# Kernel optimization log

Hardware: AMD Instinct MI355X
Metric: run time of the kernel (lower is better)

## Reference

```python
import jax, jax.numpy as jnp
import numpy as np

N_NODES = 100000
N_EDGES = 3200000
D = 128


def setup_inputs() -> dict:
    key = jax.random.key(0)
    k1, k2, k3, k4, k5 = jax.random.split(key, 5)
    x = jax.random.normal(k1, (N_NODES, D), dtype=jnp.float32)
    weight = jax.random.normal(k2, (D, D), dtype=jnp.float32) * (1.0 / np.sqrt(D))
    bias = jax.random.normal(k3, (D,), dtype=jnp.float32) * 0.01
    edge_weight = jax.random.uniform(k4, (N_EDGES,), dtype=jnp.float32)
    edge_index = jax.random.randint(k5, (2, N_EDGES), 0, N_NODES, dtype=jnp.int64 if jax.config.jax_enable_x64 else jnp.int32)
    return {"x": x, "weight": weight, "bias": bias,
            "edge_weight": edge_weight, "edge_index": edge_index}


def gcn_conv(x, weight, bias, edge_index, edge_weight):
    # PyG GCNConv defaults: normalize=True, add_self_loops=True (fill=1),
    # flow source_to_target: messages gathered from edge_index[0], scattered to edge_index[1].
    n = x.shape[0]
    src, dst = edge_index[0], edge_index[1]
    loop = jnp.arange(n, dtype=src.dtype)
    src = jnp.concatenate([src, loop])
    dst = jnp.concatenate([dst, loop])
    ew = jnp.concatenate([edge_weight, jnp.ones((n,), dtype=edge_weight.dtype)])
    deg = jax.ops.segment_sum(ew, dst, num_segments=n)          # [N]
    dinv = jnp.where(deg > 0, jax.lax.rsqrt(jnp.where(deg > 0, deg, 1.0)), 0.0)
    norm = dinv[src] * ew * dinv[dst]                           # [E+N]
    h = x @ weight.T                                            # [N, D_out]
    msg = h[src] * norm[:, None]                                # gather + scale
    out = jax.ops.segment_sum(msg, dst, num_segments=n)         # scatter-add
    return out + bias


def reference(x, weight, bias, edge_weight, edge_index):
    h = gcn_conv(x, weight, bias, edge_index, edge_weight)
    h = jax.nn.relu(h)            # normalizer is Identity, activation=F.relu
    h = h + x                     # input_dim == output_dim -> projection=Identity
    # dropout: eval mode (deterministic reference) -> no-op
    return h
```

## Files before the change

### kernel.cpp

```cpp
#include <hip/hip_runtime.h>

#define N_NODES 100000
#define N_EDGES 3200000
#define DIM 128

#define NB_C  98
#define CAP_C 36864
#define NB_F  1568
#define CAP_F 2560
#define CAP   96


typedef __attribute__((ext_vector_type(4))) float f32x4;
typedef __attribute__((ext_vector_type(8))) short s16x8;


__device__ __forceinline__ unsigned short f2bf(float f) {
    unsigned u = __float_as_uint(f);
    return (unsigned short)((u + 0x7fffu + ((u >> 16) & 1u)) >> 16);
}


__global__ __launch_bounds__(256) void zero_i_kernel(int* __restrict__ p, int n) {
    int i = blockIdx.x * 256 + threadIdx.x;
    if (i < n) p[i] = 0;
}

__global__ __launch_bounds__(256) void zero_f_kernel(float* __restrict__ p, int n) {
    int i = blockIdx.x * 256 + threadIdx.x;
    if (i < n) p[i] = 0.0f;
}

__global__ __launch_bounds__(256) void zero_u64_kernel(unsigned long long* __restrict__ p, int n) {
    int i = blockIdx.x * 256 + threadIdx.x;
    if (i < n) p[i] = 0ull;
}

__global__ __launch_bounds__(256) void zero_f4_kernel(float4* __restrict__ p, int n4) {
    int i = blockIdx.x * 256 + threadIdx.x;
    if (i < n4) p[i] = make_float4(0.f, 0.f, 0.f, 0.f);
}

__global__ __launch_bounds__(256) void dinv_kernel(float* __restrict__ deg) {
    int i = blockIdx.x * 256 + threadIdx.x;
    if (i < N_NODES) deg[i] = rsqrtf(deg[i] + 1.0f);
}

__global__ __launch_bounds__(256) void dinv_packed_kernel(const unsigned long long* __restrict__ packed,
                                                          float* __restrict__ dinv) {
    int i = blockIdx.x * 256 + threadIdx.x;
    if (i < N_NODES) {
        unsigned long long p = packed[i];
        float deg = (float)(p & 0xFFFFFFFFFFull) * (1.0f / 4294967296.0f);
        dinv[i] = rsqrtf(deg + 1.0f);
    }
}

__global__ __launch_bounds__(256) void wt_kernel(const float* __restrict__ W,
                                                 float* __restrict__ Wt) {
    int idx = blockIdx.x * 256 + threadIdx.x;
    int j = idx >> 7, k = idx & 127;
    Wt[k * 128 + j] = W[idx];
}


__global__ __launch_bounds__(256) void prep_kernel(const float* __restrict__ W,
                                                   ushort* __restrict__ wf_hi,
                                                   ushort* __restrict__ wf_lo,
                                                   int* __restrict__ fills) {
    const int b = blockIdx.x;
    const int tid = threadIdx.x;
    if (b < 64) {
        int idx  = b * 256 + tid;
        int j    = idx & 7;
        int lane = (idx >> 3) & 63;
        int ks   = (idx >> 9) & 3;
        int ct   = idx >> 11;
        int col  = ct * 16 + (lane & 15);
        int k    = ks * 32 + ((lane >> 4) << 3) + j;
        float w  = W[col * 128 + k];
        unsigned short hb = f2bf(w);
        float rem = w - __uint_as_float((unsigned)hb << 16);
        wf_hi[idx] = hb;
        wf_lo[idx] = f2bf(rem);
    } else {
        int i = (b - 64) * 256 + tid;
        if (i < NB_C + NB_F) fills[i] = 0;
    }
}


__global__ __launch_bounds__(256) void partA1_kernel(const int* __restrict__ ei,
                                                     const float* __restrict__ ew,
                                                     int* __restrict__ fill_c,
                                                     unsigned long long* __restrict__ edc) {
    __shared__ int hist[NB_C];
    __shared__ int base[NB_C];
    const int tid = threadIdx.x;
    const int blockbase = blockIdx.x * 4096;
    for (int i = tid; i < NB_C; i += 256) hist[i] = 0;
    __syncthreads();

    unsigned long long pay[16];
    unsigned meta[16];
#pragma unroll
    for (int i = 0; i < 16; ++i) {
        int e = blockbase + i * 256 + tid;
        meta[i] = 0xFFFFFFFFu;
        if (e < N_EDGES) {
            int src = ei[e];
            int dst = ei[N_EDGES + e];
            float w = ew[e];
            int cb = dst >> 10;
            int pos = atomicAdd(&hist[cb], 1);
            pay[i] = ((unsigned long long)__float_as_uint(w) << 32)
                   | ((unsigned)(dst & 1023) << 17) | (unsigned)src;
            meta[i] = ((unsigned)cb << 16) | (unsigned)pos;
        }
    }
    __syncthreads();
    for (int c = tid; c < NB_C; c += 256) {
        int cnt = hist[c];
        base[c] = (cnt > 0) ? atomicAdd(&fill_c[c], cnt) : 0;
    }
    __syncthreads();
#pragma unroll
    for (int i = 0; i < 16; ++i) {
        if (meta[i] != 0xFFFFFFFFu) {
            int cb = (int)(meta[i] >> 16);
            int pos = base[cb] + (int)(meta[i] & 0xFFFFu);
            if (pos < CAP_C)
                edc[(unsigned)cb * CAP_C + (unsigned)pos] = pay[i];
        }
    }
}


__global__ __launch_bounds__(256) void partA2_kernel(const int* __restrict__ fill_c,
                                                     const unsigned long long* __restrict__ edc,
                                                     int* __restrict__ fill_f,
                                                     unsigned long long* __restrict__ edf) {
    __shared__ int hist[16];
    __shared__ int base[16];
    const int tid = threadIdx.x;
    const int cb = blockIdx.x / 9;
    const int lo = (blockIdx.x % 9) * 4096;
    const int cnt_c = min(fill_c[cb], CAP_C);
    const int hi = min(lo + 4096, cnt_c);
    if (tid < 16) hist[tid] = 0;
    __syncthreads();

    unsigned long long pay[16];
    unsigned meta[16];
#pragma unroll
    for (int i = 0; i < 16; ++i) {
        int idx = lo + i * 256 + tid;
        meta[i] = 0xFFFFFFFFu;
        if (idx < hi) {
            unsigned long long p = edc[(unsigned)cb * CAP_C + (unsigned)idx];
            int f = (int)((p >> 23) & 15);
            int pos = atomicAdd(&hist[f], 1);
            pay[i] = p;
            meta[i] = ((unsigned)f << 16) | (unsigned)pos;
        }
    }
    __syncthreads();
    if (tid < 16) {
        int c = hist[tid];
        base[tid] = (c > 0) ? atomicAdd(&fill_f[cb * 16 + tid], c) : 0;
    }
    __syncthreads();
#pragma unroll
    for (int i = 0; i < 16; ++i) {
        if (meta[i] != 0xFFFFFFFFu) {
            int f = (int)(meta[i] >> 16);
            int pos = base[f] + (int)(meta[i] & 0xFFFFu);
            if (pos < CAP_F)
                edf[((unsigned)(cb * 16 + f)) * CAP_F + (unsigned)pos] = pay[i];
        }
    }
}


__global__ __launch_bounds__(256) void partB_kernel(const int* __restrict__ fill_f,
                                                    unsigned long long* __restrict__ edf,
                                                    float* __restrict__ dinv,
                                                    int* __restrict__ row_start,
                                                    int* __restrict__ row_cnt,
                                                    const float4* __restrict__ x4,
                                                    ushort4* __restrict__ xh4) {
    __shared__ unsigned long long hd[64];
    __shared__ int pref[64];
    __shared__ float dinv_s[64];
    const int tid = threadIdx.x;
    const int fb = blockIdx.x;
    const int node_base = fb * 64;
    const int cnt = min(fill_f[fb], CAP_F);
    if (tid < 64) hd[tid] = 0ull;
    __syncthreads();

    unsigned long long pay[10];
    unsigned meta[10];
#pragma unroll
    for (int it = 0; it < 10; ++it) {
        int idx = it * 256 + tid;
        meta[it] = 0xFFFFFFFFu;
        if (idx < cnt) {
            unsigned long long p = edf[(unsigned)fb * CAP_F + (unsigned)idx];
            int dl = (int)((p >> 17) & 63);
            float w = __uint_as_float((unsigned)(p >> 32));
            unsigned long long inc = 1ull |
                ((unsigned long long)(unsigned)(w * 16777216.0f + 0.5f) << 32);
            unsigned long long old = atomicAdd(&hd[dl], inc);
            pay[it] = p;
            meta[it] = ((unsigned)dl << 16) | (unsigned)(old & 0xFFFFull);
        }
    }
    __syncthreads();
    if (tid == 0) {
        int run = 0;
#pragma unroll
        for (int n = 0; n < 64; ++n) { pref[n] = run; run += (int)(hd[n] & 0xFFFFFFFFull); }
    }
    __syncthreads();
    if (tid < 64) {
        int node = node_base + tid;
        if (node < N_NODES) {
            float deg = (float)(unsigned)(hd[tid] >> 32) * (1.0f / 16777216.0f);
            float dv = rsqrtf(deg + 1.0f);
            dinv[node] = dv;
            dinv_s[tid] = dv;
            row_start[node] = fb * CAP_F + pref[tid];
            row_cnt[node] = (int)(hd[tid] & 0xFFFFFFFFull);
        }
    }
#pragma unroll
    for (int it = 0; it < 10; ++it) {
        if (meta[it] != 0xFFFFFFFFu) {
            int dl = (int)(meta[it] >> 16);
            edf[(unsigned)fb * CAP_F + (unsigned)(pref[dl] + (int)(meta[it] & 0xFFFFu))] = pay[it];
        }
    }
    __syncthreads();
#pragma unroll
    for (int i = 0; i < 8; ++i) {
        int idx = i * 256 + tid;
        int r = idx >> 5;
        int node = node_base + r;
        if (node < N_NODES) {
            float dv = dinv_s[r];
            float4 v = x4[(unsigned)node * 32u + (unsigned)(idx & 31)];
            ushort4 h;
            h.x = f2bf(v.x * dv); h.y = f2bf(v.y * dv);
            h.z = f2bf(v.z * dv); h.w = f2bf(v.w * dv);
            xh4[(unsigned)node * 32u + (unsigned)(idx & 31)] = h;
        }
    }
}


__global__ __launch_bounds__(256) void gatherc_kernel(const int* __restrict__ row_start,
                                                      const int* __restrict__ row_cnt,
                                                      const unsigned long long* __restrict__ edf,
                                                      const float* __restrict__ dinv,
                                                      const unsigned* __restrict__ xh,
                                                      float2* __restrict__ agg2) {
    const int lane = threadIdx.x & 63;
    const int node = blockIdx.x * 4 + (threadIdx.x >> 6);

    const int cnt = row_cnt[node];
    const int start = row_start[node];
    float ax0 = 0.f, ay0 = 0.f, ax1 = 0.f, ay1 = 0.f;

    for (int b = 0; b < cnt; b += 64) {
        int idx = b + lane;
        const bool valid = idx < cnt;
        if (!valid) idx = cnt - 1;
        unsigned long long p = edf[(unsigned)(start + idx)];
        int msrc = (int)(p & 0x1FFFFull);
        float mw = valid ? __uint_as_float((unsigned)(p >> 32)) : 0.0f;
        const int mcnt = min(64, cnt - b);
        const int ng = (mcnt + 7) >> 3;

        unsigned va[8], vb[8];

#define PREF(buf, JB)                                                          \
        _Pragma("unroll")                                                      \
        for (int j = 0; j < 8; ++j) {                                          \
            int s = __builtin_amdgcn_readlane(msrc, (JB) + j);                 \
            buf[j] = xh[(unsigned)s * 64u + (unsigned)lane];                   \
        }
#define CONSUME(buf, JB)                                                       \
        _Pragma("unroll")                                                      \
        for (int j = 0; j < 8; ++j) {                                          \
            float w = __int_as_float(                                          \
                __builtin_amdgcn_readlane(__float_as_int(mw), (JB) + j));      \
            if (j & 1) {                                                       \
                ax1 = fmaf(__uint_as_float(buf[j] << 16), w, ax1);             \
                ay1 = fmaf(__uint_as_float(buf[j] & 0xffff0000u), w, ay1);     \
            } else {                                                           \
                ax0 = fmaf(__uint_as_float(buf[j] << 16), w, ax0);             \
                ay0 = fmaf(__uint_as_float(buf[j] & 0xffff0000u), w, ay0);     \
            }                                                                  \
        }

        PREF(va, 0);
        int g = 0;
        for (; g + 2 < ng; g += 2) {
            PREF(vb, (g + 1) * 8);
            CONSUME(va, g * 8);
            PREF(va, (g + 2) * 8);
            CONSUME(vb, (g + 1) * 8);
        }
        if (g + 1 < ng) {
            PREF(vb, (g + 1) * 8);
            CONSUME(va, g * 8);
            CONSUME(vb, (g + 1) * 8);
        } else {
            CONSUME(va, g * 8);
        }
#undef PREF
#undef CONSUME
    }

    float di = dinv[node];
    agg2[(unsigned)node * 64u + lane] = make_float2((ax0 + ax1) * di, (ay0 + ay1) * di);
}


__global__ __launch_bounds__(256) void bucket_f32_kernel(const int* __restrict__ ei,
                                                         const float* __restrict__ ew,
                                                         unsigned long long* __restrict__ packed,
                                                         int2* __restrict__ ed) {
    int e = blockIdx.x * 256 + threadIdx.x;
    int src = ei[e];
    int dst = ei[N_EDGES + e];
    float w = ew[e];
    unsigned long long inc = (1ull << 40) | (unsigned long long)(w * 4294967296.0f);
    unsigned long long old = atomicAdd(&packed[dst], inc);
    unsigned slot = (unsigned)(old >> 40);
    if (slot < CAP) {
        ed[(unsigned)dst * CAP + slot] = make_int2(src, __float_as_int(w));
    }
}

__global__ __launch_bounds__(256) void gatherb_f32_kernel(const unsigned long long* __restrict__ packed,
                                                          const int2* __restrict__ ed,
                                                          const float* __restrict__ dinv,
                                                          const float2* __restrict__ x2,
                                                          float2* __restrict__ agg2) {
    const int wave = threadIdx.x >> 6;
    const int lane = threadIdx.x & 63;
    const int node = blockIdx.x * 4 + wave;

    int cnt = (int)(packed[node] >> 40);
    cnt = min(cnt, CAP);
    const unsigned base = (unsigned)node * CAP;
    float2 acc = make_float2(0.f, 0.f);

    for (int b = 0; b < cnt; b += 64) {
        int idx = b + lane;
        if (idx >= cnt) idx = cnt - 1;
        int2 my = ed[base + idx];
        float wmy = __int_as_float(my.y) * dinv[my.x];
        int m = min(64, cnt - b);
#pragma unroll 8
        for (int j = 0; j < m; ++j) {
            int s = __builtin_amdgcn_readlane(my.x, j);
            float w = __int_as_float(__builtin_amdgcn_readlane(__float_as_int(wmy), j));
            float2 v = x2[(unsigned)s * 64u + lane];
            acc.x = fmaf(v.x, w, acc.x); acc.y = fmaf(v.y, w, acc.y);
        }
    }
    float di = dinv[node];
    acc.x *= di; acc.y *= di;
    agg2[(unsigned)node * 64u + lane] = acc;
}

__global__ __launch_bounds__(256) void count_deg_kernel(const int* __restrict__ ei,
                                                        const float* __restrict__ ew,
                                                        int* __restrict__ count,
                                                        float* __restrict__ deg) {
    int e = blockIdx.x * 256 + threadIdx.x;
    int dst = ei[N_EDGES + e];
    atomicAdd(&count[dst], 1);
    atomicAdd(&deg[dst], ew[e]);
}

__global__ __launch_bounds__(256) void scatter_kernel(const int* __restrict__ ei,
                                                      const float* __restrict__ ew,
                                                      const float* __restrict__ dinv,
                                                      const float4* __restrict__ x4,
                                                      float* __restrict__ agg) {
    unsigned gid = blockIdx.x * 256u + threadIdx.x;
    unsigned e  = gid >> 5;
    unsigned f4 = gid & 31u;
    int src = ei[e];
    int dst = ei[N_EDGES + e];
    float w = dinv[src] * ew[e] * dinv[dst];
    float4 v = x4[(unsigned)src * 32u + f4];
    float* o = agg + ((unsigned)dst * 128u + f4 * 4u);
    atomicAdd(o + 0, v.x * w);
    atomicAdd(o + 1, v.y * w);
    atomicAdd(o + 2, v.z * w);
    atomicAdd(o + 3, v.w * w);
}


__global__ __launch_bounds__(256) void final_mfma_kernel(const float* __restrict__ agg_in,
                                                         const float* __restrict__ x,
                                                         const float* __restrict__ bias,
                                                         const float* __restrict__ dinv,
                                                         const ushort* __restrict__ wf_hi,
                                                         const ushort* __restrict__ wf_lo,
                                                         float* __restrict__ out) {
    __shared__ ushort sh_hi[16384];
    __shared__ ushort sh_lo[16384];
    const int tid = threadIdx.x;
    {
        const float4* sh4 = (const float4*)wf_hi;
        const float4* sl4 = (const float4*)wf_lo;
        float4* dh = (float4*)sh_hi;
        float4* dl = (float4*)sh_lo;
#pragma unroll
        for (int i = 0; i < 8; ++i) {
            dh[i * 256 + tid] = sh4[i * 256 + tid];
            dl[i * 256 + tid] = sl4[i * 256 + tid];
        }
    }
    __syncthreads();

    const int wave = tid >> 6;
    const int lane = tid & 63;
    const int r0 = blockIdx.x * 64 + wave * 16;
    const int mrow = lane & 15;
    const int kg = lane >> 4;
    const int arow = min(r0 + mrow, N_NODES - 1);
    const float di = dinv[arow];
    const float di2 = di * di;

    s16x8 ah[4], al[4];
#pragma unroll
    for (int ks = 0; ks < 4; ++ks) {
        const float* ap = agg_in + (unsigned)arow * 128u + ks * 32 + kg * 8;
        const float* xp = x      + (unsigned)arow * 128u + ks * 32 + kg * 8;
        float4 a0 = *(const float4*)ap;
        float4 a1 = *(const float4*)(ap + 4);
        float4 x0 = *(const float4*)xp;
        float4 x1 = *(const float4*)(xp + 4);
        float v[8] = {a0.x + x0.x * di2, a0.y + x0.y * di2,
                      a0.z + x0.z * di2, a0.w + x0.w * di2,
                      a1.x + x1.x * di2, a1.y + x1.y * di2,
                      a1.z + x1.z * di2, a1.w + x1.w * di2};
        s16x8 h, l;
#pragma unroll
        for (int j = 0; j < 8; ++j) {
            unsigned short hb = f2bf(v[j]);
            h[j] = (short)hb;
            l[j] = (short)f2bf(v[j] - __uint_as_float((unsigned)hb << 16));
        }
        ah[ks] = h; al[ks] = l;
    }

#pragma unroll
    for (int ct = 0; ct < 8; ++ct) {
        f32x4 acc = {0.f, 0.f, 0.f, 0.f};
#pragma unroll
        for (int ks = 0; ks < 4; ++ks) {
            const int fo = ((ct * 4 + ks) * 64 + lane) * 8;
            s16x8 bh = *(const s16x8*)&sh_hi[fo];
            s16x8 bl = *(const s16x8*)&sh_lo[fo];
            acc = __builtin_amdgcn_mfma_f32_16x16x32_bf16(ah[ks], bh, acc, 0, 0, 0);
            acc = __builtin_amdgcn_mfma_f32_16x16x32_bf16(ah[ks], bl, acc, 0, 0, 0);
            acc = __builtin_amdgcn_mfma_f32_16x16x32_bf16(al[ks], bh, acc, 0, 0, 0);
        }
        const int col = ct * 16 + mrow;
        const float bv = bias[col];
#pragma unroll
        for (int v = 0; v < 4; ++v) {
            const int row = r0 + kg * 4 + v;
            if (row < N_NODES) {
                float o = fmaxf(acc[v] + bv, 0.f) + x[(unsigned)row * 128u + col];
                out[(unsigned)row * 128u + col] = o;
            }
        }
    }
}


__global__ __launch_bounds__(256) void final_kernel(const float* __restrict__ agg_in,
                                                    const float* __restrict__ x,
                                                    const float* __restrict__ bias,
                                                    const float* __restrict__ dinv,
                                                    const float* __restrict__ Wt,
                                                    float* __restrict__ out) {
    __shared__ float sh_wt[16384];
    const int tid = threadIdx.x;
    {
        const float4* s4 = (const float4*)Wt;
        float4* d4 = (float4*)sh_wt;
#pragma unroll
        for (int i = 0; i < 16; ++i) d4[i * 256 + tid] = s4[i * 256 + tid];
    }
    __syncthreads();

    const int wave = tid >> 6;
    const int lane = tid & 63;
    const int rowbase = blockIdx.x * 32 + wave * 8;

    float areg[16];
#pragma unroll
    for (int r = 0; r < 8; ++r) {
        int row = rowbase + r;
        float di = dinv[row];
        float di2 = di * di;
        int base = row * 128;
        areg[2 * r]     = agg_in[base + lane]      + x[base + lane]      * di2;
        areg[2 * r + 1] = agg_in[base + 64 + lane] + x[base + 64 + lane] * di2;
    }

    float acc0[8], acc1[8];
#pragma unroll
    for (int r = 0; r < 8; ++r) { acc0[r] = 0.f; acc1[r] = 0.f; }

    const float2* wt2 = (const float2*)sh_wt;

#pragma unroll
    for (int kh = 0; kh < 2; ++kh) {
#pragma unroll 16
        for (int kk = 0; kk < 64; ++kk) {
            int k = kh * 64 + kk;
            float2 w = wt2[k * 64 + lane];
#pragma unroll
            for (int r = 0; r < 8; ++r) {
                float ak = __uint_as_float(
                    __builtin_amdgcn_readlane(__float_as_uint(areg[2 * r + kh]), kk));
                acc0[r] = fmaf(ak, w.x, acc0[r]);
                acc1[r] = fmaf(ak, w.y, acc1[r]);
            }
        }
    }

    float2 b = ((const float2*)bias)[lane];
#pragma unroll
    for (int r = 0; r < 8; ++r) {
        int row = rowbase + r;
        float2 xr = ((const float2*)x)[row * 64 + lane];
        float v0 = fmaxf(acc0[r] + b.x, 0.f) + xr.x;
        float v1 = fmaxf(acc1[r] + b.y, 0.f) + xr.y;
        ((float2*)out)[row * 64 + lane] = make_float2(v0, v1);
    }
}


extern "C" void kernel_launch(void* const* d_in, const int* in_sizes, int n_in,
                              void* d_out, int out_size, void* d_ws, size_t ws_size,
                              hipStream_t stream) {
    const float* x    = (const float*)d_in[0];
    const float* W    = (const float*)d_in[1];
    const float* bias = (const float*)d_in[2];
    const float* ew   = (const float*)d_in[3];
    const int*   ei   = (const int*)d_in[4];
    float* out = (float*)d_out;
    char* ws = (char*)d_ws;

    unsigned short* xhA  = (unsigned short*)ws;
    ushort* wfhi     = (ushort*)(ws + 25600000);
    ushort* wflo     = wfhi + 16384;
    float* dinvA     = (float*)(ws + 25665536);
    int*   row_start = (int*)  (ws + 26065536);
    int*   row_cnt   = (int*)  (ws + 26465536);
    int*   fill_c    = (int*)  (ws + 26865536);
    int*   fill_f    = fill_c + NB_C;
    unsigned long long* edc = (unsigned long long*)(ws + 26872256);
    unsigned long long* edf = (unsigned long long*)(ws + 55773632);
    const size_t WS_PART = 87886272ull;

    unsigned long long* packed = (unsigned long long*)ws;
    float* dinvB = (float*)(ws + 800000);
    float* WtB   = (float*)(ws + 1200000);
    int2*  edB   = (int2*)(ws + 1265536);
    const size_t WS_BUCKET = 1265536ull + (size_t)N_NODES * CAP * 8ull;

    if (ws_size >= WS_PART) {
        prep_kernel<<<71, 256, 0, stream>>>(W, wfhi, wflo, fill_c);
        partA1_kernel<<<(N_EDGES + 4095) / 4096, 256, 0, stream>>>(ei, ew, fill_c, edc);
        partA2_kernel<<<NB_C * 9, 256, 0, stream>>>(fill_c, edc, fill_f, edf);
        partB_kernel<<<NB_F, 256, 0, stream>>>(fill_f, edf, dinvA, row_start, row_cnt,
                                               (const float4*)x, (ushort4*)xhA);
        gatherc_kernel<<<N_NODES / 4, 256, 0, stream>>>(row_start, row_cnt, edf, dinvA,
                                                        (const unsigned*)xhA, (float2*)out);
        final_mfma_kernel<<<(N_NODES + 63) / 64, 256, 0, stream>>>(out, x, bias, dinvA,
                                                                   wfhi, wflo, out);
    } else if (ws_size >= WS_BUCKET) {
        zero_u64_kernel<<<(N_NODES + 255) / 256, 256, 0, stream>>>(packed, N_NODES);
        wt_kernel<<<64, 256, 0, stream>>>(W, WtB);
        bucket_f32_kernel<<<N_EDGES / 256, 256, 0, stream>>>(ei, ew, packed, edB);
        dinv_packed_kernel<<<(N_NODES + 255) / 256, 256, 0, stream>>>(packed, dinvB);
        gatherb_f32_kernel<<<N_NODES / 4, 256, 0, stream>>>(packed, edB, dinvB,
                                                            (const float2*)x, (float2*)out);
        final_kernel<<<N_NODES / 32, 256, 0, stream>>>(out, x, bias, dinvB, WtB, out);
    } else {
        float* deg   = (float*)(ws);
        float* Wt    = (float*)(ws + 400000);
        int*   count = (int*)  (ws + 465536);
        zero_f_kernel<<<(N_NODES + 255) / 256, 256, 0, stream>>>(deg, N_NODES);
        zero_i_kernel<<<(N_NODES + 255) / 256, 256, 0, stream>>>(count, N_NODES);
        wt_kernel<<<64, 256, 0, stream>>>(W, Wt);
        zero_f4_kernel<<<(N_NODES * DIM / 4) / 256, 256, 0, stream>>>((float4*)out,
                                                                      N_NODES * DIM / 4);
        count_deg_kernel<<<N_EDGES / 256, 256, 0, stream>>>(ei, ew, count, deg);
        dinv_kernel<<<(N_NODES + 255) / 256, 256, 0, stream>>>(deg);
        scatter_kernel<<<(N_EDGES / 256) * 32, 256, 0, stream>>>(ei, ew, deg,
                                                                 (const float4*)x, out);
        final_kernel<<<N_NODES / 32, 256, 0, stream>>>(out, x, bias, deg, Wt, out);
    }
}
```

Measured before the change: 351.7 us.

## Replace two-level edge partition with single 256-node bucket pass and staged writes

The three-stage bucketing of edges by destination (1024-node coarse buckets, then 64-node fine buckets, then per-node sort) becomes two stages. A1 now bins edges into 391 buckets of 256 nodes and stages them contiguously in shared memory so the global writes come out grouped per bucket. partB2 then does the per-node histogram and sort directly for each 256-node bucket, and one full pass over the edge list goes away. The final MFMA kernel also stops copying the split-bf16 weights into LDS and reads them straight from global memory. The cost is fewer, larger blocks in partB2 (391), serial loops over up to about 9k edges per block, and B-fragment loads that now depend on cache.

```diff
diff --git a/kernel.cpp b/kernel.cpp
--- a/kernel.cpp
+++ b/kernel.cpp
@@ -4,10 +4,8 @@
 #define N_EDGES 3200000
 #define DIM 128
 
-#define NB_C  98
-#define CAP_C 36864
-#define NB_F  1568
-#define CAP_F 2560
+#define NB2   391
+#define CAP2  9216
 #define CAP   96
 
 
@@ -85,7 +83,7 @@
         wf_lo[idx] = f2bf(rem);
     } else {
         int i = (b - 64) * 256 + tid;
-        if (i < NB_C + NB_F) fills[i] = 0;
+        if (i < NB2) fills[i] = 0;
     }
 }
 
@@ -94,11 +92,15 @@
                                                      const float* __restrict__ ew,
                                                      int* __restrict__ fill_c,
                                                      unsigned long long* __restrict__ edc) {
-    __shared__ int hist[NB_C];
-    __shared__ int base[NB_C];
+    __shared__ int hist[NB2];
+    __shared__ int base[NB2];
+    __shared__ int lpref[NB2 + 1];
+    __shared__ int stripe[98];
+    __shared__ unsigned long long stage[4096];
+    __shared__ unsigned short segid[4096];
     const int tid = threadIdx.x;
     const int blockbase = blockIdx.x * 4096;
-    for (int i = tid; i < NB_C; i += 256) hist[i] = 0;
+    for (int i = tid; i < NB2; i += 256) hist[i] = 0;
     __syncthreads();
 
     unsigned long long pay[16];
@@ -111,139 +113,138 @@
             int src = ei[e];
             int dst = ei[N_EDGES + e];
             float w = ew[e];
-            int cb = dst >> 10;
+            int cb = dst >> 8;
             int pos = atomicAdd(&hist[cb], 1);
             pay[i] = ((unsigned long long)__float_as_uint(w) << 32)
-                   | ((unsigned)(dst & 1023) << 17) | (unsigned)src;
+                   | ((unsigned)(dst & 255) << 17) | (unsigned)src;
             meta[i] = ((unsigned)cb << 16) | (unsigned)pos;
         }
     }
     __syncthreads();
-    for (int c = tid; c < NB_C; c += 256) {
+    for (int c = tid; c < NB2; c += 256) {
         int cnt = hist[c];
         base[c] = (cnt > 0) ? atomicAdd(&fill_c[c], cnt) : 0;
+    }
+    if (tid < 98) {
+        int s = 0;
+#pragma unroll
+        for (int k = 0; k < 4; ++k) { int c = tid * 4 + k; if (c < NB2) s += hist[c]; }
+        stripe[tid] = s;
+    }
+    __syncthreads();
+    if (tid == 0) {
+        int run = 0;
+#pragma unroll
+        for (int i = 0; i < 98; ++i) { int t = stripe[i]; stripe[i] = run; run += t; }
+        lpref[NB2] = run;
+    }
+    __syncthreads();
+    if (tid < 98) {
+        int run = stripe[tid];
+#pragma unroll
+        for (int k = 0; k < 4; ++k) {
+            int c = tid * 4 + k;
+            if (c < NB2) { lpref[c] = run; run += hist[c]; }
+        }
     }
     __syncthreads();
 #pragma unroll
     for (int i = 0; i < 16; ++i) {
         if (meta[i] != 0xFFFFFFFFu) {
             int cb = (int)(meta[i] >> 16);
-            int pos = base[cb] + (int)(meta[i] & 0xFFFFu);
-            if (pos < CAP_C)
-                edc[(unsigned)cb * CAP_C + (unsigned)pos] = pay[i];
-        }
-    }
-}
-
-
-__global__ __launch_bounds__(256) void partA2_kernel(const int* __restrict__ fill_c,
+            int slot = lpref[cb] + (int)(meta[i] & 0xFFFFu);
+            stage[slot] = pay[i];
+            segid[slot] = (unsigned short)cb;
+        }
+    }
+    __syncthreads();
+    const int total = lpref[NB2];
+#pragma unroll
+    for (int r = 0; r < 16; ++r) {
+        int i = r * 256 + tid;
+        if (i < total) {
+            int sid = segid[i];
+            int g = base[sid] + (i - lpref[sid]);
+            if (g < CAP2)
+                edc[(unsigned)sid * CAP2 + (unsigned)g] = stage[i];
+        }
+    }
+}
+
+
+__global__ __launch_bounds__(256) void partB2_kernel(const int* __restrict__ fill_c,
                                                      const unsigned long long* __restrict__ edc,
-                                                     int* __restrict__ fill_f,
-                                                     unsigned long long* __restrict__ edf) {
-    __shared__ int hist[16];
-    __shared__ int base[16];
-    const int tid = threadIdx.x;
-    const int cb = blockIdx.x / 9;
-    const int lo = (blockIdx.x % 9) * 4096;
-    const int cnt_c = min(fill_c[cb], CAP_C);
-    const int hi = min(lo + 4096, cnt_c);
-    if (tid < 16) hist[tid] = 0;
-    __syncthreads();
-
-    unsigned long long pay[16];
-    unsigned meta[16];
-#pragma unroll
-    for (int i = 0; i < 16; ++i) {
-        int idx = lo + i * 256 + tid;
-        meta[i] = 0xFFFFFFFFu;
-        if (idx < hi) {
-            unsigned long long p = edc[(unsigned)cb * CAP_C + (unsigned)idx];
-            int f = (int)((p >> 23) & 15);
-            int pos = atomicAdd(&hist[f], 1);
-            pay[i] = p;
-            meta[i] = ((unsigned)f << 16) | (unsigned)pos;
-        }
-    }
-    __syncthreads();
-    if (tid < 16) {
-        int c = hist[tid];
-        base[tid] = (c > 0) ? atomicAdd(&fill_f[cb * 16 + tid], c) : 0;
-    }
-    __syncthreads();
-#pragma unroll
-    for (int i = 0; i < 16; ++i) {
-        if (meta[i] != 0xFFFFFFFFu) {
-            int f = (int)(meta[i] >> 16);
-            int pos = base[f] + (int)(meta[i] & 0xFFFFu);
-            if (pos < CAP_F)
-                edf[((unsigned)(cb * 16 + f)) * CAP_F + (unsigned)pos] = pay[i];
-        }
-    }
-}
-
-
-__global__ __launch_bounds__(256) void partB_kernel(const int* __restrict__ fill_f,
-                                                    unsigned long long* __restrict__ edf,
-                                                    float* __restrict__ dinv,
-                                                    int* __restrict__ row_start,
-                                                    int* __restrict__ row_cnt,
-                                                    const float4* __restrict__ x4,
-                                                    ushort4* __restrict__ xh4) {
-    __shared__ unsigned long long hd[64];
-    __shared__ int pref[64];
-    __shared__ float dinv_s[64];
+                                                     unsigned long long* __restrict__ edf,
+                                                     float* __restrict__ dinv,
+                                                     int* __restrict__ row_start,
+                                                     int* __restrict__ row_cnt,
+                                                     const float4* __restrict__ x4,
+                                                     ushort4* __restrict__ xh4) {
+    __shared__ unsigned long long hd[256];
+    __shared__ int pref[256];
+    __shared__ int alloc_[256];
+    __shared__ int stripe[64];
+    __shared__ float dinv_s[256];
     const int tid = threadIdx.x;
     const int fb = blockIdx.x;
-    const int node_base = fb * 64;
-    const int cnt = min(fill_f[fb], CAP_F);
-    if (tid < 64) hd[tid] = 0ull;
-    __syncthreads();
-
-    unsigned long long pay[10];
-    unsigned meta[10];
-#pragma unroll
-    for (int it = 0; it < 10; ++it) {
-        int idx = it * 256 + tid;
-        meta[it] = 0xFFFFFFFFu;
-        if (idx < cnt) {
-            unsigned long long p = edf[(unsigned)fb * CAP_F + (unsigned)idx];
-            int dl = (int)((p >> 17) & 63);
-            float w = __uint_as_float((unsigned)(p >> 32));
-            unsigned long long inc = 1ull |
-                ((unsigned long long)(unsigned)(w * 16777216.0f + 0.5f) << 32);
-            unsigned long long old = atomicAdd(&hd[dl], inc);
-            pay[it] = p;
-            meta[it] = ((unsigned)dl << 16) | (unsigned)(old & 0xFFFFull);
-        }
+    const int node_base = fb * 256;
+    const int cnt = min(fill_c[fb], CAP2);
+    const unsigned ebase = (unsigned)fb * CAP2;
+    hd[tid] = 0ull;
+    __syncthreads();
+
+    for (int idx = tid; idx < cnt; idx += 256) {
+        unsigned long long p = edc[ebase + (unsigned)idx];
+        int dl = (int)((p >> 17) & 255);
+        float w = __uint_as_float((unsigned)(p >> 32));
+        unsigned long long inc = 1ull |
+            ((unsigned long long)(unsigned)(w * 16777216.0f + 0.5f) << 32);
+        atomicAdd(&hd[dl], inc);
+    }
+    __syncthreads();
+    if (tid < 64) {
+        int s = 0;
+#pragma unroll
+        for (int k = 0; k < 4; ++k) s += (int)(hd[tid * 4 + k] & 0xFFFFFFFFull);
+        stripe[tid] = s;
     }
     __syncthreads();
     if (tid == 0) {
         int run = 0;
 #pragma unroll
-        for (int n = 0; n < 64; ++n) { pref[n] = run; run += (int)(hd[n] & 0xFFFFFFFFull); }
+        for (int i = 0; i < 64; ++i) { int t = stripe[i]; stripe[i] = run; run += t; }
     }
     __syncthreads();
     if (tid < 64) {
+        int run = stripe[tid];
+#pragma unroll
+        for (int k = 0; k < 4; ++k) {
+            pref[tid * 4 + k] = run;
+            run += (int)(hd[tid * 4 + k] & 0xFFFFFFFFull);
+        }
+    }
+    __syncthreads();
+    {
         int node = node_base + tid;
         if (node < N_NODES) {
             float deg = (float)(unsigned)(hd[tid] >> 32) * (1.0f / 16777216.0f);
             float dv = rsqrtf(deg + 1.0f);
             dinv[node] = dv;
             dinv_s[tid] = dv;
-            row_start[node] = fb * CAP_F + pref[tid];
+            row_start[node] = (int)(ebase + (unsigned)pref[tid]);
             row_cnt[node] = (int)(hd[tid] & 0xFFFFFFFFull);
         }
-    }
-#pragma unroll
-    for (int it = 0; it < 10; ++it) {
-        if (meta[it] != 0xFFFFFFFFu) {
-            int dl = (int)(meta[it] >> 16);
-            edf[(unsigned)fb * CAP_F + (unsigned)(pref[dl] + (int)(meta[it] & 0xFFFFu))] = pay[it];
-        }
-    }
-    __syncthreads();
-#pragma unroll
-    for (int i = 0; i < 8; ++i) {
+        alloc_[tid] = pref[tid];
+    }
+    __syncthreads();
+    for (int idx = tid; idx < cnt; idx += 256) {
+        unsigned long long p = edc[ebase + (unsigned)idx];
+        int dl = (int)((p >> 17) & 255);
+        int pos = atomicAdd(&alloc_[dl], 1);
+        edf[ebase + (unsigned)pos] = p;
+    }
+#pragma unroll
+    for (int i = 0; i < 32; ++i) {
         int idx = i * 256 + tid;
         int r = idx >> 5;
         int node = node_base + r;
@@ -414,22 +415,7 @@
                                                          const ushort* __restrict__ wf_hi,
                                                          const ushort* __restrict__ wf_lo,
                                                          float* __restrict__ out) {
-    __shared__ ushort sh_hi[16384];
-    __shared__ ushort sh_lo[16384];
     const int tid = threadIdx.x;
-    {
-        const float4* sh4 = (const float4*)wf_hi;
-        const float4* sl4 = (const float4*)wf_lo;
-        float4* dh = (float4*)sh_hi;
-        float4* dl = (float4*)sh_lo;
-#pragma unroll
-        for (int i = 0; i < 8; ++i) {
-            dh[i * 256 + tid] = sh4[i * 256 + tid];
-            dl[i * 256 + tid] = sl4[i * 256 + tid];
-        }
-    }
-    __syncthreads();
-
     const int wave = tid >> 6;
     const int lane = tid & 63;
     const int r0 = blockIdx.x * 64 + wave * 16;
@@ -468,8 +454,8 @@
 #pragma unroll
         for (int ks = 0; ks < 4; ++ks) {
             const int fo = ((ct * 4 + ks) * 64 + lane) * 8;
-            s16x8 bh = *(const s16x8*)&sh_hi[fo];
-            s16x8 bl = *(const s16x8*)&sh_lo[fo];
+            s16x8 bh = *(const s16x8*)&wf_hi[fo];
+            s16x8 bl = *(const s16x8*)&wf_lo[fo];
             acc = __builtin_amdgcn_mfma_f32_16x16x32_bf16(ah[ks], bh, acc, 0, 0, 0);
             acc = __builtin_amdgcn_mfma_f32_16x16x32_bf16(ah[ks], bl, acc, 0, 0, 0);
             acc = __builtin_amdgcn_mfma_f32_16x16x32_bf16(al[ks], bh, acc, 0, 0, 0);
@@ -571,7 +557,6 @@
     int*   row_start = (int*)  (ws + 26065536);
     int*   row_cnt   = (int*)  (ws + 26465536);
     int*   fill_c    = (int*)  (ws + 26865536);
-    int*   fill_f    = fill_c + NB_C;
     unsigned long long* edc = (unsigned long long*)(ws + 26872256);
     unsigned long long* edf = (unsigned long long*)(ws + 55773632);
     const size_t WS_PART = 87886272ull;
@@ -583,10 +568,9 @@
     const size_t WS_BUCKET = 1265536ull + (size_t)N_NODES * CAP * 8ull;
 
     if (ws_size >= WS_PART) {
-        prep_kernel<<<71, 256, 0, stream>>>(W, wfhi, wflo, fill_c);
+        prep_kernel<<<66, 256, 0, stream>>>(W, wfhi, wflo, fill_c);
         partA1_kernel<<<(N_EDGES + 4095) / 4096, 256, 0, stream>>>(ei, ew, fill_c, edc);
-        partA2_kernel<<<NB_C * 9, 256, 0, stream>>>(fill_c, edc, fill_f, edf);
-        partB_kernel<<<NB_F, 256, 0, stream>>>(fill_f, edf, dinvA, row_start, row_cnt,
+        partB2_kernel<<<NB2, 256, 0, stream>>>(fill_c, edc, edf, dinvA, row_start, row_cnt,
                                                (const float4*)x, (ushort4*)xhA);
         gatherc_kernel<<<N_NODES / 4, 256, 0, stream>>>(row_start, row_cnt, edf, dinvA,
                                                         (const unsigned*)xhA, (float2*)out);
```

Measured after the change: 371.1 us. 5.5% more time.
